# Kernel optimization log

Measured on AMD Instinct MI355X. Metric: run time of the kernel, lower is better.

## Reference

```python
import jax, jax.numpy as jnp
import numpy as np

B, N, M = 8, 4096, 4096

def _sqdist(x, y):
    # x: [B,N,3], y: [B,M,3] -> squared euclidean distances [B,N,M]
    return jnp.sum((x[:, :, None, :] - y[:, None, :, :]) ** 2, axis=-1)

def _approx_match(xyz1, xyz2):
    # Faithful port of Fan et al. approxmatch.cu (used by PyTorchEMD's
    # earth_mover_distance): annealed soft-assignment over 10 levels.
    b, n, _ = xyz1.shape
    m = xyz2.shape[1]
    d2 = _sqdist(xyz1, xyz2)                      # [B,N,M]
    factorl = max(n, m) / n
    factorr = max(n, m) / m
    satl = jnp.full((b, n), factorl, d2.dtype)    # remaining mass, left
    satr = jnp.full((b, m), factorr, d2.dtype)    # remaining mass, right
    match = jnp.zeros_like(d2)
    # levels: -4^7 .. -4^-1, then 0 (exactly as in approxmatch.cu)
    levels = [-(4.0 ** j) for j in range(7, -2, -1)] + [0.0]
    for level in levels:
        w = jnp.exp(level * d2) * satr[:, None, :]                 # [B,N,M]
        w = w * (satl / (jnp.sum(w, axis=2) + 1e-9))[:, :, None]   # row normalize
        ss2 = jnp.sum(w, axis=1)                                   # [B,M]
        ratio = jnp.minimum(satr / (ss2 + 1e-9), 1.0)
        w = w * ratio[:, None, :]                                  # col capacity clamp
        match = match + w
        satl = jnp.maximum(satl - jnp.sum(w, axis=2), 0.0)
        satr = jnp.maximum(satr - ss2 * ratio, 0.0)
    return match, d2

def setup_inputs() -> dict:
    key = jax.random.key(0)
    k1, k2 = jax.random.split(key)
    array1 = jax.random.uniform(k1, (B, N, 3), dtype=jnp.float32)
    array2 = jax.random.uniform(k2, (B, M, 3), dtype=jnp.float32)
    return {"array1": array1, "array2": array2}

def reference(array1, array2):
    match, d2 = _approx_match(array1, array2)
    dist = jnp.sum(match * d2, axis=(1, 2))   # per-batch EMD (squared-dist transport cost), [B]
    return jnp.mean(dist) / array1.shape[1]
```

## Files before the change

kernel.cpp:

```cpp
#include <hip/hip_runtime.h>


#define BB 8
#define NN 4096
#define MM 4096
#define NPTS 4096

constexpr int BLK   = 256;
constexpr int S     = 16;
constexpr int R     = 4;
constexpr int RPB   = (BLK / S) * R;
constexpr int CHUNK = 2048;
constexpr int G     = (CHUNK / S) / 4;

#if defined(__has_builtin)
#if __has_builtin(__builtin_amdgcn_exp2f)
#define EXP2F(x) __builtin_amdgcn_exp2f(x)
#endif
#if __has_builtin(__builtin_amdgcn_logf)
#define LOG2F(x) __builtin_amdgcn_logf(x)
#endif
#endif
#ifndef EXP2F
#define EXP2F(x) exp2f(x)
#endif
#ifndef LOG2F
#define LOG2F(x) log2f(x)
#endif

__global__ void emd_sort(const float* __restrict__ xyz, float* __restrict__ xyzs) {
    __shared__ int hist[64];
    __shared__ int offs[64];
    __shared__ int cur[64];
    const int b = blockIdx.x;
    const float* src = xyz + (size_t)b * NPTS * 3;
    float* dst = xyzs + (size_t)b * NPTS * 3;
    for (int i = threadIdx.x; i < 64; i += BLK) hist[i] = 0;
    __syncthreads();
    for (int i = threadIdx.x; i < NPTS; i += BLK) {
        float x = src[3*i], y = src[3*i+1], z = src[3*i+2];
        int cx = (int)(x * 4.0f); cx = cx < 0 ? 0 : (cx > 3 ? 3 : cx);
        int cy = (int)(y * 4.0f); cy = cy < 0 ? 0 : (cy > 3 ? 3 : cy);
        int cz = (int)(z * 4.0f); cz = cz < 0 ? 0 : (cz > 3 ? 3 : cz);
        atomicAdd(&hist[(cx << 4) | (cy << 2) | cz], 1);
    }
    __syncthreads();
    if (threadIdx.x == 0) {
        int acc = 0;
        for (int k = 0; k < 64; ++k) { offs[k] = acc; cur[k] = acc; acc += hist[k]; }
    }
    __syncthreads();
    for (int i = threadIdx.x; i < NPTS; i += BLK) {
        float x = src[3*i], y = src[3*i+1], z = src[3*i+2];
        int cx = (int)(x * 4.0f); cx = cx < 0 ? 0 : (cx > 3 ? 3 : cx);
        int cy = (int)(y * 4.0f); cy = cy < 0 ? 0 : (cy > 3 ? 3 : cy);
        int cz = (int)(z * 4.0f); cz = cz < 0 ? 0 : (cz > 3 ? 3 : cz);
        int idx = atomicAdd(&cur[(cx << 4) | (cy << 2) | cz], 1);
        dst[3*idx] = x; dst[3*idx+1] = y; dst[3*idx+2] = z;
    }
}

__global__ void emd_bbox(const float* __restrict__ xyzs, float* __restrict__ bb,
                         int gp) {
    const int grp = blockIdx.x, lane = threadIdx.x;
    float xlo = 1e30f, xhi = -1e30f, ylo = 1e30f, yhi = -1e30f,
          zlo = 1e30f, zhi = -1e30f;
    if (lane < gp) {
        const float* p = xyzs + ((size_t)grp * gp + lane) * 3;
        xlo = xhi = p[0]; ylo = yhi = p[1]; zlo = zhi = p[2];
    }
    #pragma unroll
    for (int d = 1; d < 64; d <<= 1) {
        xlo = fminf(xlo, __shfl_xor(xlo, d)); xhi = fmaxf(xhi, __shfl_xor(xhi, d));
        ylo = fminf(ylo, __shfl_xor(ylo, d)); yhi = fmaxf(yhi, __shfl_xor(yhi, d));
        zlo = fminf(zlo, __shfl_xor(zlo, d)); zhi = fmaxf(zhi, __shfl_xor(zhi, d));
    }
    if (lane == 0) {
        float* o = bb + (size_t)grp * 6;
        o[0]=xlo; o[1]=xhi; o[2]=ylo; o[3]=yhi; o[4]=zlo; o[5]=zhi;
    }
}

__global__ void emd_init(float* __restrict__ satl, float* __restrict__ satr,
                         float* __restrict__ bsum, float* __restrict__ slsum,
                         float* __restrict__ scal, float* __restrict__ out) {
    int i = blockIdx.x * blockDim.x + threadIdx.x;
    if (i < BB * NN) satl[i] = 1.0f;
    if (i < BB * MM) satr[i] = 1.0f;
    if (i < BB)      bsum[i] = 0.0f;
    if (i < BB)      slsum[i] = 0.0f;
    if (i < BB * 5)  scal[i] = 0.0f;
    if (i == 0)      out[0]  = 0.0f;
}

#define AB_LOAD(vv, gg)                                          \
    _Pragma("unroll")                                            \
    for (int k = 0; k < 4; ++k) vv[k] = q[((gg)*4 + k)*S + s];

#define AB_COMP(vv)                                              \
    _Pragma("unroll")                                            \
    for (int k = 0; k < 4; ++k) {                                \
        float4 v = vv[k];                                        \
        _Pragma("unroll")                                        \
        for (int r = 0; r < R; ++r) {                            \
            float a0 = v.w + cpp[r];                             \
            float a1 = fmaf(zs[r], v.z, a0);                     \
            float a2 = fmaf(ys[r], v.y, a1);                     \
            float arg = fmaf(xs[r], v.x, a2);                    \
            acc[r] += EXP2F(arg);                                \
        }                                                        \
    }

#define RED_S(v)                                                 \
    v += __shfl_xor(v, 1);  v += __shfl_xor(v, 2);               \
    v += __shfl_xor(v, 4);  v += __shfl_xor(v, 8);

#define RED_W(v)                                                 \
    v += __shfl_xor(v, 1);  v += __shfl_xor(v, 2);               \
    v += __shfl_xor(v, 4);  v += __shfl_xor(v, 8);               \
    v += __shfl_xor(v, 16); v += __shfl_xor(v, 32);

#define BOX_SETUP(rbb)                                           \
    const float* rb = (rbb) + (size_t)(b * 256 + tile * 4 + (threadIdx.x >> 6)) * 6; \
    const float rx0 = rb[0], rx1 = rb[1], ry0 = rb[2], ry1 = rb[3], \
                rz0 = rb[4], rz1 = rb[5];

#define BOX_D2M(cbb, c0, gs, d2m)                                \
    const float* cb = (cbb) + (size_t)(b * 64 + ((c0) >> 6) + (gs)) * 6; \
    float gx = fmaxf(0.0f, fmaxf(cb[0] - rx1, rx0 - cb[1]));     \
    float gy = fmaxf(0.0f, fmaxf(cb[2] - ry1, ry0 - cb[3]));     \
    float gz = fmaxf(0.0f, fmaxf(cb[4] - rz1, rz0 - cb[5]));     \
    float d2m = fmaf(gx, gx, fmaf(gy, gy, gz * gz));

__global__ __launch_bounds__(BLK, 2) void emd_passA_p(
        const float* __restrict__ xyz1, const float* __restrict__ xyz2,
        const float* __restrict__ satl, const float* __restrict__ satr,
        float* __restrict__ sl, const float* __restrict__ rbb,
        const float* __restrict__ cbb, float c, float T) {
    __shared__ float4 q[CHUNK];
    const int b    = blockIdx.x / (NN / RPB);
    const int tile = blockIdx.x % (NN / RPB);
    const float* x2b = xyz2 + (size_t)b * MM * 3;
    const float* srb = satr + (size_t)b * MM;

    const int g = threadIdx.x / S, s = threadIdx.x % S;
    const int n0 = tile * RPB + g * R;
    const float* p = xyz1 + ((size_t)b * NN + n0) * 3;
    const float m2c = -2.0f * c;
    float xs[R], ys[R], zs[R], cpp[R], acc[R];
    #pragma unroll
    for (int r = 0; r < R; ++r) {
        float x = p[3*r], y = p[3*r+1], z = p[3*r+2];
        cpp[r] = c * (x*x + y*y + z*z);
        xs[r] = m2c * x; ys[r] = m2c * y; zs[r] = m2c * z;
        acc[r] = 0.0f;
    }
    BOX_SETUP(rbb);

    for (int c0 = 0; c0 < MM; c0 += CHUNK) {
        __syncthreads();
        for (int m = threadIdx.x; m < CHUNK; m += BLK) {
            int mm = c0 + m;
            float xx = x2b[3*mm], yy = x2b[3*mm+1], zz = x2b[3*mm+2];
            float qq = xx*xx + yy*yy + zz*zz;
            q[m] = make_float4(xx, yy, zz, fmaf(c, qq, LOG2F(srb[mm])));
        }
        __syncthreads();
        for (int gs = 0; gs < G; ++gs) {
            BOX_D2M(cbb, c0, gs, d2m);
            if (d2m > T) continue;
            float4 va[4];
            AB_LOAD(va, gs);
            AB_COMP(va);
        }
    }
    #pragma unroll
    for (int r = 0; r < R; ++r) { RED_S(acc[r]); }
    if (s == 0) {
        #pragma unroll
        for (int r = 0; r < R; ++r) {
            int gi = b * NN + n0 + r;
            sl[gi] = satl[gi] / (acc[r] + 1e-9f);
        }
    }
}

template<int PRUNE>
__global__ __launch_bounds__(BLK, 2) void emd_passB(
        const float* __restrict__ xyz1, const float* __restrict__ xyz2,
        const float* __restrict__ sl, float* __restrict__ satr,
        float* __restrict__ sr2, float* __restrict__ bsum,
        const float* __restrict__ rbb, const float* __restrict__ cbb,
        int do_sum, float c, float T) {
    __shared__ float4 q[CHUNK];
    const int b    = blockIdx.x / (MM / RPB);
    const int tile = blockIdx.x % (MM / RPB);
    const float* x1b = xyz1 + (size_t)b * NN * 3;
    const float* slb = sl + (size_t)b * NN;

    const int g = threadIdx.x / S, s = threadIdx.x % S;
    const int m0 = tile * RPB + g * R;
    const float* qp = xyz2 + ((size_t)b * MM + m0) * 3;
    const float m2c = -2.0f * c;
    float xs[R], ys[R], zs[R], cpp[R], acc[R];
    #pragma unroll
    for (int r = 0; r < R; ++r) {
        float x = qp[3*r], y = qp[3*r+1], z = qp[3*r+2];
        cpp[r] = c * (x*x + y*y + z*z);
        xs[r] = m2c * x; ys[r] = m2c * y; zs[r] = m2c * z;
        acc[r] = 0.0f;
    }
    BOX_SETUP(rbb);

    for (int c0 = 0; c0 < NN; c0 += CHUNK) {
        __syncthreads();
        for (int n = threadIdx.x; n < CHUNK; n += BLK) {
            int nn = c0 + n;
            float xx = x1b[3*nn], yy = x1b[3*nn+1], zz = x1b[3*nn+2];
            float pp = xx*xx + yy*yy + zz*zz;
            q[n] = make_float4(xx, yy, zz, fmaf(c, pp, LOG2F(slb[nn])));
        }
        __syncthreads();
        if (PRUNE) {
            for (int gs = 0; gs < G; ++gs) {
                BOX_D2M(cbb, c0, gs, d2m);
                if (d2m > T) continue;
                float4 va[4];
                AB_LOAD(va, gs);
                AB_COMP(va);
            }
        } else {
            float4 va[4], vb[4];
            AB_LOAD(va, 0);
            #pragma unroll 1
            for (int gs = 0; gs < G; gs += 2) {
                AB_LOAD(vb, gs + 1);
                AB_COMP(va);
                if (gs + 2 < G) { AB_LOAD(va, gs + 2); }
                AB_COMP(vb);
            }
        }
    }
    #pragma unroll
    for (int r = 0; r < R; ++r) { RED_S(acc[r]); }
    float part = 0.0f;
    if (s == 0) {
        #pragma unroll
        for (int r = 0; r < R; ++r) {
            int gi = b * MM + m0 + r;
            float sr    = satr[gi];
            float ss2   = acc[r] * sr;
            float ratio = fminf(sr / (ss2 + 1e-9f), 1.0f);
            float sn    = fmaxf(sr - ss2 * ratio, 0.0f);
            sr2[gi]  = sr * ratio;
            satr[gi] = sn;
            part += sn;
        }
    }
    if (do_sum) {
        RED_W(part);
        if ((threadIdx.x & 63) == 0) atomicAdd(&bsum[b], part);
    }
}

#define CA0_LOAD(vv, ww, gg)                                     \
    _Pragma("unroll")                                            \
    for (int k = 0; k < 4; ++k) {                                \
        int idx = ((gg)*4 + k)*S + s;                            \
        vv[k] = q[idx]; ww[k] = w[idx];                          \
    }

#define CA0_COMP(vv, ww)                                         \
    _Pragma("unroll")                                            \
    for (int k = 0; k < 4; ++k) {                                \
        float4 v = vv[k]; float2 wv = ww[k];                     \
        _Pragma("unroll")                                        \
        for (int r = 0; r < R; ++r) {                            \
            float a0 = v.w + cnpp[r];                            \
            float a1 = fmaf(zs[r], v.z, a0);                     \
            float a2 = fmaf(ys[r], v.y, a1);                     \
            float arg = fmaf(xs[r], v.x, a2);                    \
            float en  = EXP2F(arg);                              \
            acc2[r] = fmaf(en, wv.y, acc2[r]);                   \
            float e2 = en * en;                                  \
            float t  = (e2 * e2) * wv.x;                         \
            rd[r]   += t;                                        \
            costA[r] = fmaf(t, arg, costA[r]);                   \
        }                                                        \
    }

template<int PRUNE>
__global__ __launch_bounds__(BLK, 2) void emd_passCA0(
        const float* __restrict__ xyz1, const float* __restrict__ xyz2,
        float* __restrict__ sl, float* __restrict__ satl,
        const float* __restrict__ sr2, const float* __restrict__ satr_next,
        float* __restrict__ out, const float* __restrict__ rbb,
        const float* __restrict__ cbb, float cl, float cn, float T) {
    __shared__ float4 q[CHUNK];
    __shared__ float2 w[CHUNK];
    const int b    = blockIdx.x / (NN / RPB);
    const int tile = blockIdx.x % (NN / RPB);
    const float* x2b = xyz2 + (size_t)b * MM * 3;
    const float* s2b = sr2 + (size_t)b * MM;
    const float* srb = satr_next + (size_t)b * MM;

    const int g = threadIdx.x / S, s = threadIdx.x % S;
    const int n0 = tile * RPB + g * R;
    const float* pp_ = xyz1 + ((size_t)b * NN + n0) * 3;
    const float m2cn = -2.0f * cn;
    const float icn  = 1.0f / cn;
    float xs[R], ys[R], zs[R], cnpp[R], rd[R], costA[R], acc2[R], slv[R];
    #pragma unroll
    for (int r = 0; r < R; ++r) {
        float x = pp_[3*r], y = pp_[3*r+1], z = pp_[3*r+2];
        cnpp[r] = cn * (x*x + y*y + z*z);
        xs[r] = m2cn * x; ys[r] = m2cn * y; zs[r] = m2cn * z;
        rd[r] = 0.0f; costA[r] = 0.0f; acc2[r] = 0.0f;
        slv[r] = sl[b * NN + n0 + r];
    }
    BOX_SETUP(rbb);

    for (int c0 = 0; c0 < MM; c0 += CHUNK) {
        __syncthreads();
        for (int m = threadIdx.x; m < CHUNK; m += BLK) {
            int mm = c0 + m;
            float xx = x2b[3*mm], yy = x2b[3*mm+1], zz = x2b[3*mm+2];
            float qq = xx*xx + yy*yy + zz*zz;
            q[m] = make_float4(xx, yy, zz, cn * qq);
            w[m] = make_float2(s2b[mm], srb[mm]);
        }
        __syncthreads();

        if (PRUNE) {
            for (int gs = 0; gs < G; ++gs) {
                BOX_D2M(cbb, c0, gs, d2m);
                if (d2m > T) continue;
                float4 va[4]; float2 wa[4];
                CA0_LOAD(va, wa, gs);
                CA0_COMP(va, wa);
            }
        } else {
            float4 va[4], vb[4]; float2 wa[4], wb[4];
            CA0_LOAD(va, wa, 0);
            #pragma unroll 1
            for (int gs = 0; gs < G; gs += 2) {
                CA0_LOAD(vb, wb, gs + 1);
                CA0_COMP(va, wa);
                if (gs + 2 < G) { CA0_LOAD(va, wa, gs + 2); }
                CA0_COMP(vb, wb);
            }
        }
    }

    #pragma unroll
    for (int r = 0; r < R; ++r) { RED_S(rd[r]); RED_S(acc2[r]); }

    float csum = 0.0f;
    #pragma unroll
    for (int r = 0; r < R; ++r) csum += (costA[r] * icn) * slv[r];
    RED_W(csum);
    if ((threadIdx.x & 63) == 0)
        atomicAdd(out, csum * (1.0f / (float)(BB * NN)));

    if (s == 0) {
        #pragma unroll
        for (int r = 0; r < R; ++r) {
            int gi = b * NN + n0 + r;
            float sa = fmaxf(satl[gi] - rd[r] * slv[r], 0.0f);
            satl[gi] = sa;
            sl[gi] = sa / (acc2[r] + 1e-9f);
        }
    }
}

#define CA1_LOAD(vv, aa, gg)                                     \
    _Pragma("unroll")                                            \
    for (int k = 0; k < 4; ++k) {                                \
        int idx = ((gg)*4 + k)*S + s;                            \
        vv[k] = q[idx]; aa[k] = qa[idx];                         \
    }

#define CA1_COMP(vv, aa)                                         \
    _Pragma("unroll")                                            \
    for (int k = 0; k < 4; ++k) {                                \
        float4 v = vv[k]; float lw = aa[k];                      \
        _Pragma("unroll")                                        \
        for (int r = 0; r < R; ++r) {                            \
            float a0 = v.w + clpp[r];                            \
            float a1 = fmaf(zs[r], v.z, a0);                     \
            float a2 = fmaf(ys[r], v.y, a1);                     \
            float arg = fmaf(xs[r], v.x, a2);                    \
            float t   = EXP2F(arg);                              \
            rd[r] += t;                                          \
            c1[r] = fmaf(t, arg, c1[r]);                         \
            c2[r] = fmaf(t, lw, c2[r]);                          \
        }                                                        \
    }

__global__ __launch_bounds__(BLK, 2) void emd_passCA1(
        const float* __restrict__ xyz1, const float* __restrict__ xyz2,
        float* __restrict__ sl, float* __restrict__ satl,
        const float* __restrict__ sr2, const float* __restrict__ bsum,
        float* __restrict__ slsum, float* __restrict__ out, float cl) {
    __shared__ float4 q[CHUNK];
    __shared__ float  qa[CHUNK];
    const int b    = blockIdx.x / (NN / RPB);
    const int tile = blockIdx.x % (NN / RPB);
    const float* x2b = xyz2 + (size_t)b * MM * 3;
    const float* s2b = sr2 + (size_t)b * MM;

    const int g = threadIdx.x / S, s = threadIdx.x % S;
    const int n0 = tile * RPB + g * R;
    const float* pp_ = xyz1 + ((size_t)b * NN + n0) * 3;
    const float m2cl = -2.0f * cl;
    const float icl  = 1.0f / cl;
    float xs[R], ys[R], zs[R], clpp[R], rd[R], c1[R], c2[R], slv[R];
    #pragma unroll
    for (int r = 0; r < R; ++r) {
        float x = pp_[3*r], y = pp_[3*r+1], z = pp_[3*r+2];
        clpp[r] = cl * (x*x + y*y + z*z);
        xs[r] = m2cl * x; ys[r] = m2cl * y; zs[r] = m2cl * z;
        rd[r] = 0.0f; c1[r] = 0.0f; c2[r] = 0.0f;
        slv[r] = sl[b * NN + n0 + r];
    }

    for (int c0 = 0; c0 < MM; c0 += CHUNK) {
        __syncthreads();
        for (int m = threadIdx.x; m < CHUNK; m += BLK) {
            int mm = c0 + m;
            float xx = x2b[3*mm], yy = x2b[3*mm+1], zz = x2b[3*mm+2];
            float qq = xx*xx + yy*yy + zz*zz;
            float lw = LOG2F(fmaxf(s2b[mm], 1e-30f));
            q[m]  = make_float4(xx, yy, zz, fmaf(cl, qq, lw));
            qa[m] = lw;
        }
        __syncthreads();

        float4 va[4], vb[4]; float aa[4], ab[4];
        CA1_LOAD(va, aa, 0);
        #pragma unroll 1
        for (int gs = 0; gs < G; gs += 2) {
            CA1_LOAD(vb, ab, gs + 1);
            CA1_COMP(va, aa);
            if (gs + 2 < G) { CA1_LOAD(va, aa, gs + 2); }
            CA1_COMP(vb, ab);
        }
    }

    #pragma unroll
    for (int r = 0; r < R; ++r) { RED_S(rd[r]); }

    float csum = 0.0f;
    #pragma unroll
    for (int r = 0; r < R; ++r) csum += ((c1[r] - c2[r]) * icl) * slv[r];
    RED_W(csum);
    if ((threadIdx.x & 63) == 0)
        atomicAdd(out, csum * (1.0f / (float)(BB * NN)));

    float part = 0.0f;
    if (s == 0) {
        float bs = bsum[b];
        #pragma unroll
        for (int r = 0; r < R; ++r) {
            int gi = b * NN + n0 + r;
            float sa = fmaxf(satl[gi] - rd[r] * slv[r], 0.0f);
            satl[gi] = sa;
            float s9 = sa / (bs + 1e-9f);
            sl[gi] = s9;
            part += s9;
        }
    }
    RED_W(part);
    if ((threadIdx.x & 63) == 0) atomicAdd(&slsum[b], part);
}

__global__ void emd_lvl9_col(const float* __restrict__ xyz2,
                             const float* __restrict__ satr,
                             const float* __restrict__ slsum,
                             float* __restrict__ scal) {
    int i = blockIdx.x * blockDim.x + threadIdx.x;
    int b = i / MM;
    const float* qp = xyz2 + (size_t)i * 3;
    float sr = satr[i];
    float ss2 = sr * slsum[b];
    float ratio = fminf(sr / (ss2 + 1e-9f), 1.0f);
    float s2 = sr * ratio;
    float x = qp[0], y = qp[1], z = qp[2];
    float v0 = s2, v1 = s2*x, v2 = s2*y, v3 = s2*z;
    float v4 = s2 * (x*x + y*y + z*z);
    #pragma unroll
    for (int d = 1; d < 64; d <<= 1) {
        v0 += __shfl_xor(v0, d); v1 += __shfl_xor(v1, d);
        v2 += __shfl_xor(v2, d); v3 += __shfl_xor(v3, d);
        v4 += __shfl_xor(v4, d);
    }
    if ((threadIdx.x & 63) == 0) {
        atomicAdd(&scal[b*5+0], v0); atomicAdd(&scal[b*5+1], v1);
        atomicAdd(&scal[b*5+2], v2); atomicAdd(&scal[b*5+3], v3);
        atomicAdd(&scal[b*5+4], v4);
    }
}

__global__ void emd_lvl9_cost(const float* __restrict__ xyz1,
                              const float* __restrict__ sl,
                              const float* __restrict__ scal,
                              float* __restrict__ out) {
    int i = blockIdx.x * blockDim.x + threadIdx.x;
    int b = i / NN;
    float W  = scal[b*5+0], Wx = scal[b*5+1], Wy = scal[b*5+2];
    float Wz = scal[b*5+3], Q  = scal[b*5+4];
    const float* p = xyz1 + (size_t)i * 3;
    float x = p[0], y = p[1], z = p[2];
    float pp = x*x + y*y + z*z;
    float dotw = x*Wx + y*Wy + z*Wz;
    float c = sl[i] * (pp * W + Q - 2.0f * dotw);
    #pragma unroll
    for (int d = 1; d < 64; d <<= 1) c += __shfl_xor(c, d);
    if ((threadIdx.x & 63) == 0)
        atomicAdd(out, c * (1.0f / (float)(BB * NN)));
}

extern "C" void kernel_launch(void* const* d_in, const int* in_sizes, int n_in,
                              void* d_out, int out_size, void* d_ws, size_t ws_size,
                              hipStream_t stream) {
    const float* xyz1 = (const float*)d_in[0];
    const float* xyz2 = (const float*)d_in[1];
    float* out  = (float*)d_out;

    float* satl  = (float*)d_ws;
    float* sl    = satl  + BB * NN;
    float* satr  = sl    + BB * NN;
    float* sr2   = satr  + BB * MM;
    float* bsum  = sr2   + BB * MM;
    float* slsum = bsum  + BB;
    float* scal  = slsum + BB;
    float* xyz1s = scal  + BB * 5;
    float* xyz2s = xyz1s + BB * NN * 3;
    float* bb1_16 = xyz2s + BB * MM * 3;
    float* bb1_64 = bb1_16 + BB * 256 * 6;
    float* bb2_16 = bb1_64 + BB * 64 * 6;
    float* bb2_64 = bb2_16 + BB * 256 * 6;

    emd_sort<<<BB, BLK, 0, stream>>>(xyz1, xyz1s);
    emd_sort<<<BB, BLK, 0, stream>>>(xyz2, xyz2s);
    emd_bbox<<<BB * (NN / 16), 64, 0, stream>>>(xyz1s, bb1_16, 16);
    emd_bbox<<<BB * (NN / 64), 64, 0, stream>>>(xyz1s, bb1_64, 64);
    emd_bbox<<<BB * (MM / 16), 64, 0, stream>>>(xyz2s, bb2_16, 16);
    emd_bbox<<<BB * (MM / 64), 64, 0, stream>>>(xyz2s, bb2_64, 64);
    emd_init<<<(BB * NN + 255) / 256, 256, 0, stream>>>(satl, satr, bsum,
                                                        slsum, scal, out);

    const double levels[10] = {-16384.0, -4096.0, -1024.0, -256.0, -64.0,
                               -16.0, -4.0, -1.0, -0.25, 0.0};
    const double LOG2E = 1.4426950408889634;
    float c[10], T[10];
    for (int l = 0; l < 10; ++l) {
        c[l] = (float)(levels[l] * LOG2E);
        T[l] = (l < 9) ? (float)(80.0 / (-levels[l] * LOG2E)) : 1e30f;
    }

    const int grid = BB * (NN / RPB);

    emd_passA_p<<<grid, BLK, 0, stream>>>(xyz1s, xyz2s, satl, satr, sl,
                                          bb1_16, bb2_64, c[0], T[0]);
    for (int l = 0; l <= 8; ++l) {
        if (l <= 3)
            emd_passB<1><<<grid, BLK, 0, stream>>>(
                xyz1s, xyz2s, sl, satr, sr2, bsum, bb2_16, bb1_64, 0, c[l], T[l]);
        else
            emd_passB<0><<<grid, BLK, 0, stream>>>(
                xyz1s, xyz2s, sl, satr, sr2, bsum, bb2_16, bb1_64,
                (l == 8) ? 1 : 0, c[l], 1e30f);
        if (l <= 2)
            emd_passCA0<1><<<grid, BLK, 0, stream>>>(
                xyz1s, xyz2s, sl, satl, sr2, satr, out, bb1_16, bb2_64,
                c[l], c[l + 1], T[l + 1]);
        else if (l < 8)
            emd_passCA0<0><<<grid, BLK, 0, stream>>>(
                xyz1s, xyz2s, sl, satl, sr2, satr, out, bb1_16, bb2_64,
                c[l], c[l + 1], 1e30f);
        else
            emd_passCA1<<<grid, BLK, 0, stream>>>(
                xyz1s, xyz2s, sl, satl, sr2, bsum, slsum, out, c[l]);
    }
    emd_lvl9_col<<<BB * MM / 256, 256, 0, stream>>>(xyz2s, satr, slsum, scal);
    emd_lvl9_cost<<<BB * NN / 256, 256, 0, stream>>>(xyz1s, sl, scal, out);
}
```

Measured before the change: 856.6 us.

## Compact saturated rows and columns out of the dense annealing levels

Adds compaction kernels that gather the points whose remaining mass is above a small threshold into packed float4 buffers with index maps. Levels 3 to 8 then run new passB/passCA0/passCA1 variants over only the active rows and columns, and blocks past the active count return early. Nearly-saturated points contribute almost no work, so this aims to cut the O(N·M) exp work in the later levels. In exchange it adds two compaction launches per level, indirect scatter writes, and a small approximation from treating mass below 1e-8 as zero.

```diff
diff --git a/kernel.cpp b/kernel.cpp
--- a/kernel.cpp
+++ b/kernel.cpp
@@ -6,12 +6,13 @@
 #define MM 4096
 #define NPTS 4096
 
-constexpr int BLK   = 256;
-constexpr int S     = 16;
-constexpr int R     = 4;
-constexpr int RPB   = (BLK / S) * R;
-constexpr int CHUNK = 2048;
-constexpr int G     = (CHUNK / S) / 4;
+constexpr int   BLK   = 256;
+constexpr int   S     = 16;
+constexpr int   R     = 4;
+constexpr int   RPB   = (BLK / S) * R;
+constexpr int   CHUNK = 2048;
+constexpr int   G     = (CHUNK / S) / 4;
+constexpr float TAU   = 1e-8f;
 
 #if defined(__has_builtin)
 #if __has_builtin(__builtin_amdgcn_exp2f)
@@ -30,7 +31,6 @@
 
 __global__ void emd_sort(const float* __restrict__ xyz, float* __restrict__ xyzs) {
     __shared__ int hist[64];
-    __shared__ int offs[64];
     __shared__ int cur[64];
     const int b = blockIdx.x;
     const float* src = xyz + (size_t)b * NPTS * 3;
@@ -47,7 +47,7 @@
     __syncthreads();
     if (threadIdx.x == 0) {
         int acc = 0;
-        for (int k = 0; k < 64; ++k) { offs[k] = acc; cur[k] = acc; acc += hist[k]; }
+        for (int k = 0; k < 64; ++k) { cur[k] = acc; acc += hist[k]; }
     }
     __syncthreads();
     for (int i = threadIdx.x; i < NPTS; i += BLK) {
@@ -91,6 +91,88 @@
     if (i < BB)      slsum[i] = 0.0f;
     if (i < BB * 5)  scal[i] = 0.0f;
     if (i == 0)      out[0]  = 0.0f;
+}
+
+__global__ void compact_rows(const float* __restrict__ xyzs,
+                             const float* __restrict__ satl,
+                             float* __restrict__ sl,
+                             float4* __restrict__ rowBuf, int* __restrict__ rIdx,
+                             int* __restrict__ rCnt) {
+    __shared__ int cnts[BLK];
+    const int b = blockIdx.x;
+    const int PER = NN / BLK;
+    const float* sb  = satl + (size_t)b * NN;
+    float*       slb = sl   + (size_t)b * NN;
+    const float* xb  = xyzs + (size_t)b * NN * 3;
+    const int st = threadIdx.x * PER;
+    int c = 0;
+    for (int i = 0; i < PER; ++i) c += (sb[st + i] > TAU) ? 1 : 0;
+    cnts[threadIdx.x] = c;
+    __syncthreads();
+    for (int d = 1; d < BLK; d <<= 1) {
+        int v = cnts[threadIdx.x];
+        int u = (threadIdx.x >= d) ? cnts[threadIdx.x - d] : 0;
+        __syncthreads();
+        cnts[threadIdx.x] = v + u;
+        __syncthreads();
+    }
+    const int total = cnts[BLK - 1];
+    int off = cnts[threadIdx.x] - c;
+    for (int i = 0; i < PER; ++i) {
+        int n = st + i;
+        if (sb[n] > TAU) {
+            rowBuf[(size_t)b * NN + off] =
+                make_float4(xb[3*n], xb[3*n+1], xb[3*n+2], slb[n]);
+            rIdx[(size_t)b * NN + off] = n;
+            ++off;
+        } else if (slb[n] != 0.0f) {
+            slb[n] = 0.0f;
+        }
+    }
+    for (int i = total + threadIdx.x; i < NN; i += BLK) {
+        rowBuf[(size_t)b * NN + i] = make_float4(0.f, 0.f, 0.f, 0.f);
+        rIdx[(size_t)b * NN + i] = 0;
+    }
+    if (threadIdx.x == 0) rCnt[b] = total;
+}
+
+__global__ void compact_cols(const float* __restrict__ xyzs,
+                             const float* __restrict__ satr,
+                             float4* __restrict__ colBuf, int* __restrict__ cIdx,
+                             int* __restrict__ cCnt) {
+    __shared__ int cnts[BLK];
+    const int b = blockIdx.x;
+    const int PER = MM / BLK;
+    const float* sb = satr + (size_t)b * MM;
+    const float* xb = xyzs + (size_t)b * MM * 3;
+    const int st = threadIdx.x * PER;
+    int c = 0;
+    for (int i = 0; i < PER; ++i) c += (sb[st + i] > TAU) ? 1 : 0;
+    cnts[threadIdx.x] = c;
+    __syncthreads();
+    for (int d = 1; d < BLK; d <<= 1) {
+        int v = cnts[threadIdx.x];
+        int u = (threadIdx.x >= d) ? cnts[threadIdx.x - d] : 0;
+        __syncthreads();
+        cnts[threadIdx.x] = v + u;
+        __syncthreads();
+    }
+    const int total = cnts[BLK - 1];
+    int off = cnts[threadIdx.x] - c;
+    for (int i = 0; i < PER; ++i) {
+        int m = st + i;
+        if (sb[m] > TAU) {
+            colBuf[(size_t)b * MM + off] =
+                make_float4(xb[3*m], xb[3*m+1], xb[3*m+2], sb[m]);
+            cIdx[(size_t)b * MM + off] = m;
+            ++off;
+        }
+    }
+    for (int i = total + threadIdx.x; i < MM; i += BLK) {
+        colBuf[(size_t)b * MM + i] = make_float4(0.f, 0.f, 0.f, 0.f);
+        cIdx[(size_t)b * MM + i] = 0;
+    }
+    if (threadIdx.x == 0) cCnt[b] = total;
 }
 
 #define AB_LOAD(vv, gg)                                          \
@@ -185,13 +267,11 @@
     }
 }
 
-template<int PRUNE>
-__global__ __launch_bounds__(BLK, 2) void emd_passB(
+__global__ __launch_bounds__(BLK, 2) void emd_passB_p(
         const float* __restrict__ xyz1, const float* __restrict__ xyz2,
         const float* __restrict__ sl, float* __restrict__ satr,
-        float* __restrict__ sr2, float* __restrict__ bsum,
-        const float* __restrict__ rbb, const float* __restrict__ cbb,
-        int do_sum, float c, float T) {
+        float* __restrict__ sr2, const float* __restrict__ rbb,
+        const float* __restrict__ cbb, float c, float T) {
     __shared__ float4 q[CHUNK];
     const int b    = blockIdx.x / (MM / RPB);
     const int tile = blockIdx.x % (MM / RPB);
@@ -221,29 +301,16 @@
             q[n] = make_float4(xx, yy, zz, fmaf(c, pp, LOG2F(slb[nn])));
         }
         __syncthreads();
-        if (PRUNE) {
-            for (int gs = 0; gs < G; ++gs) {
-                BOX_D2M(cbb, c0, gs, d2m);
-                if (d2m > T) continue;
-                float4 va[4];
-                AB_LOAD(va, gs);
-                AB_COMP(va);
-            }
-        } else {
-            float4 va[4], vb[4];
-            AB_LOAD(va, 0);
-            #pragma unroll 1
-            for (int gs = 0; gs < G; gs += 2) {
-                AB_LOAD(vb, gs + 1);
-                AB_COMP(va);
-                if (gs + 2 < G) { AB_LOAD(va, gs + 2); }
-                AB_COMP(vb);
-            }
+        for (int gs = 0; gs < G; ++gs) {
+            BOX_D2M(cbb, c0, gs, d2m);
+            if (d2m > T) continue;
+            float4 va[4];
+            AB_LOAD(va, gs);
+            AB_COMP(va);
         }
     }
     #pragma unroll
     for (int r = 0; r < R; ++r) { RED_S(acc[r]); }
-    float part = 0.0f;
     if (s == 0) {
         #pragma unroll
         for (int r = 0; r < R; ++r) {
@@ -254,12 +321,7 @@
             float sn    = fmaxf(sr - ss2 * ratio, 0.0f);
             sr2[gi]  = sr * ratio;
             satr[gi] = sn;
-            part += sn;
-        }
-    }
-    if (do_sum) {
-        RED_W(part);
-        if ((threadIdx.x & 63) == 0) atomicAdd(&bsum[b], part);
+        }
     }
 }
 
@@ -289,8 +351,7 @@
         }                                                        \
     }
 
-template<int PRUNE>
-__global__ __launch_bounds__(BLK, 2) void emd_passCA0(
+__global__ __launch_bounds__(BLK, 2) void emd_passCA0_p(
         const float* __restrict__ xyz1, const float* __restrict__ xyz2,
         float* __restrict__ sl, float* __restrict__ satl,
         const float* __restrict__ sr2, const float* __restrict__ satr_next,
@@ -330,25 +391,12 @@
             w[m] = make_float2(s2b[mm], srb[mm]);
         }
         __syncthreads();
-
-        if (PRUNE) {
-            for (int gs = 0; gs < G; ++gs) {
-                BOX_D2M(cbb, c0, gs, d2m);
-                if (d2m > T) continue;
-                float4 va[4]; float2 wa[4];
-                CA0_LOAD(va, wa, gs);
-                CA0_COMP(va, wa);
-            }
-        } else {
-            float4 va[4], vb[4]; float2 wa[4], wb[4];
-            CA0_LOAD(va, wa, 0);
-            #pragma unroll 1
-            for (int gs = 0; gs < G; gs += 2) {
-                CA0_LOAD(vb, wb, gs + 1);
-                CA0_COMP(va, wa);
-                if (gs + 2 < G) { CA0_LOAD(va, wa, gs + 2); }
-                CA0_COMP(vb, wb);
-            }
+        for (int gs = 0; gs < G; ++gs) {
+            BOX_D2M(cbb, c0, gs, d2m);
+            if (d2m > T) continue;
+            float4 va[4]; float2 wa[4];
+            CA0_LOAD(va, wa, gs);
+            CA0_COMP(va, wa);
         }
     }
 
@@ -369,6 +417,167 @@
             float sa = fmaxf(satl[gi] - rd[r] * slv[r], 0.0f);
             satl[gi] = sa;
             sl[gi] = sa / (acc2[r] + 1e-9f);
+        }
+    }
+}
+
+__global__ __launch_bounds__(BLK, 2) void emd_passB_c(
+        const float4* __restrict__ colBuf, const int* __restrict__ cIdx,
+        const int* __restrict__ cCnt, const float4* __restrict__ rowBuf,
+        const int* __restrict__ rCnt, float* __restrict__ satr,
+        float* __restrict__ sr2c, float* __restrict__ satrnc,
+        float* __restrict__ bsum, int do_sum, float c) {
+    __shared__ float4 q[CHUNK];
+    const int b    = blockIdx.x / (MM / RPB);
+    const int tile = blockIdx.x % (MM / RPB);
+    const int Mc = cCnt[b], Nc = rCnt[b];
+    if (tile * RPB >= Mc) return;
+    const float4* rb = rowBuf + (size_t)b * NN;
+
+    const int g = threadIdx.x / S, s = threadIdx.x % S;
+    const int m0 = tile * RPB + g * R;
+    const float m2c = -2.0f * c;
+    float xs[R], ys[R], zs[R], cpp[R], acc[R], srv[R];
+    #pragma unroll
+    for (int r = 0; r < R; ++r) {
+        float4 cv = colBuf[(size_t)b * MM + m0 + r];
+        srv[r] = cv.w;
+        cpp[r] = c * (cv.x*cv.x + cv.y*cv.y + cv.z*cv.z);
+        xs[r] = m2c * cv.x; ys[r] = m2c * cv.y; zs[r] = m2c * cv.z;
+        acc[r] = 0.0f;
+    }
+
+    const int nch = (Nc + CHUNK - 1) / CHUNK;
+    for (int ci = 0; ci < nch; ++ci) {
+        const int c0 = ci * CHUNK;
+        __syncthreads();
+        for (int n = threadIdx.x; n < CHUNK; n += BLK) {
+            int nn = c0 + n;
+            if (nn < Nc) {
+                float4 rv = rb[nn];
+                float pp = rv.x*rv.x + rv.y*rv.y + rv.z*rv.z;
+                q[n] = make_float4(rv.x, rv.y, rv.z, fmaf(c, pp, LOG2F(rv.w)));
+            } else {
+                q[n] = make_float4(0.f, 0.f, 0.f, -1e30f);
+            }
+        }
+        __syncthreads();
+        int rem = Nc - c0; if (rem > CHUNK) rem = CHUNK;
+        const int Gact = (rem + S*4 - 1) / (S*4);
+        float4 va[4], vb[4];
+        AB_LOAD(va, 0);
+        #pragma unroll 1
+        for (int gs = 0; gs < Gact; gs += 2) {
+            if (gs + 1 < Gact) { AB_LOAD(vb, gs + 1); }
+            AB_COMP(va);
+            if (gs + 2 < Gact) { AB_LOAD(va, gs + 2); }
+            if (gs + 1 < Gact) { AB_COMP(vb); }
+        }
+    }
+    #pragma unroll
+    for (int r = 0; r < R; ++r) { RED_S(acc[r]); }
+    float part = 0.0f;
+    if (s == 0) {
+        #pragma unroll
+        for (int r = 0; r < R; ++r) {
+            if (m0 + r < Mc) {
+                float sr    = srv[r];
+                float ss2   = acc[r] * sr;
+                float ratio = fminf(sr / (ss2 + 1e-9f), 1.0f);
+                float sn    = fmaxf(sr - ss2 * ratio, 0.0f);
+                size_t ci2 = (size_t)b * MM + m0 + r;
+                sr2c[ci2]   = sr * ratio;
+                satrnc[ci2] = sn;
+                satr[(size_t)b * MM + cIdx[ci2]] = sn;
+                part += sn;
+            }
+        }
+    }
+    if (do_sum) {
+        RED_W(part);
+        if ((threadIdx.x & 63) == 0) atomicAdd(&bsum[b], part);
+    }
+}
+
+__global__ __launch_bounds__(BLK, 2) void emd_passCA0_c(
+        const float4* __restrict__ rowBuf, const int* __restrict__ rIdx,
+        const int* __restrict__ rCnt, const float4* __restrict__ colBuf,
+        const int* __restrict__ cCnt, const float* __restrict__ sr2c,
+        const float* __restrict__ satrnc, float* __restrict__ satl,
+        float* __restrict__ sl, float* __restrict__ out, float cl, float cn) {
+    __shared__ float4 q[CHUNK];
+    __shared__ float2 w[CHUNK];
+    const int b    = blockIdx.x / (NN / RPB);
+    const int tile = blockIdx.x % (NN / RPB);
+    const int Nc = rCnt[b], Mc = cCnt[b];
+    if (tile * RPB >= Nc) return;
+    const float4* cbp = colBuf + (size_t)b * MM;
+    const float* s2p = sr2c + (size_t)b * MM;
+    const float* snp = satrnc + (size_t)b * MM;
+
+    const int g = threadIdx.x / S, s = threadIdx.x % S;
+    const int n0 = tile * RPB + g * R;
+    const float m2cn = -2.0f * cn;
+    const float icn  = 1.0f / cn;
+    float xs[R], ys[R], zs[R], cnpp[R], rd[R], costA[R], acc2[R], slv[R];
+    #pragma unroll
+    for (int r = 0; r < R; ++r) {
+        float4 rv = rowBuf[(size_t)b * NN + n0 + r];
+        slv[r] = rv.w;
+        cnpp[r] = cn * (rv.x*rv.x + rv.y*rv.y + rv.z*rv.z);
+        xs[r] = m2cn * rv.x; ys[r] = m2cn * rv.y; zs[r] = m2cn * rv.z;
+        rd[r] = 0.0f; costA[r] = 0.0f; acc2[r] = 0.0f;
+    }
+
+    const int nch = (Mc + CHUNK - 1) / CHUNK;
+    for (int ci = 0; ci < nch; ++ci) {
+        const int c0 = ci * CHUNK;
+        __syncthreads();
+        for (int m = threadIdx.x; m < CHUNK; m += BLK) {
+            int mm = c0 + m;
+            if (mm < Mc) {
+                float4 cv = cbp[mm];
+                float qq = cv.x*cv.x + cv.y*cv.y + cv.z*cv.z;
+                q[m] = make_float4(cv.x, cv.y, cv.z, cn * qq);
+                w[m] = make_float2(s2p[mm], snp[mm]);
+            } else {
+                q[m] = make_float4(0.f, 0.f, 0.f, 0.f);
+                w[m] = make_float2(0.f, 0.f);
+            }
+        }
+        __syncthreads();
+        int rem = Mc - c0; if (rem > CHUNK) rem = CHUNK;
+        const int Gact = (rem + S*4 - 1) / (S*4);
+        float4 va[4], vb[4]; float2 wa[4], wb[4];
+        CA0_LOAD(va, wa, 0);
+        #pragma unroll 1
+        for (int gs = 0; gs < Gact; gs += 2) {
+            if (gs + 1 < Gact) { CA0_LOAD(vb, wb, gs + 1); }
+            CA0_COMP(va, wa);
+            if (gs + 2 < Gact) { CA0_LOAD(va, wa, gs + 2); }
+            if (gs + 1 < Gact) { CA0_COMP(vb, wb); }
+        }
+    }
+
+    #pragma unroll
+    for (int r = 0; r < R; ++r) { RED_S(rd[r]); RED_S(acc2[r]); }
+
+    float csum = 0.0f;
+    #pragma unroll
+    for (int r = 0; r < R; ++r) csum += (costA[r] * icn) * slv[r];
+    RED_W(csum);
+    if ((threadIdx.x & 63) == 0)
+        atomicAdd(out, csum * (1.0f / (float)(BB * NN)));
+
+    if (s == 0) {
+        #pragma unroll
+        for (int r = 0; r < R; ++r) {
+            if (n0 + r < Nc) {
+                int gi = b * NN + rIdx[(size_t)b * NN + n0 + r];
+                float sa = fmaxf(satl[gi] - rd[r] * slv[r], 0.0f);
+                satl[gi] = sa;
+                sl[gi] = sa / (acc2[r] + 1e-9f);
+            }
         }
     }
 }
@@ -397,53 +606,64 @@
         }                                                        \
     }
 
-__global__ __launch_bounds__(BLK, 2) void emd_passCA1(
-        const float* __restrict__ xyz1, const float* __restrict__ xyz2,
-        float* __restrict__ sl, float* __restrict__ satl,
-        const float* __restrict__ sr2, const float* __restrict__ bsum,
-        float* __restrict__ slsum, float* __restrict__ out, float cl) {
+__global__ __launch_bounds__(BLK, 2) void emd_passCA1_c(
+        const float4* __restrict__ rowBuf, const int* __restrict__ rIdx,
+        const int* __restrict__ rCnt, const float4* __restrict__ colBuf,
+        const int* __restrict__ cCnt, const float* __restrict__ sr2c,
+        float* __restrict__ satl, float* __restrict__ sl,
+        const float* __restrict__ bsum, float* __restrict__ slsum,
+        float* __restrict__ out, float cl) {
     __shared__ float4 q[CHUNK];
     __shared__ float  qa[CHUNK];
     const int b    = blockIdx.x / (NN / RPB);
     const int tile = blockIdx.x % (NN / RPB);
-    const float* x2b = xyz2 + (size_t)b * MM * 3;
-    const float* s2b = sr2 + (size_t)b * MM;
+    const int Nc = rCnt[b], Mc = cCnt[b];
+    if (tile * RPB >= Nc) return;
+    const float4* cbp = colBuf + (size_t)b * MM;
+    const float* s2p = sr2c + (size_t)b * MM;
 
     const int g = threadIdx.x / S, s = threadIdx.x % S;
     const int n0 = tile * RPB + g * R;
-    const float* pp_ = xyz1 + ((size_t)b * NN + n0) * 3;
     const float m2cl = -2.0f * cl;
     const float icl  = 1.0f / cl;
     float xs[R], ys[R], zs[R], clpp[R], rd[R], c1[R], c2[R], slv[R];
     #pragma unroll
     for (int r = 0; r < R; ++r) {
-        float x = pp_[3*r], y = pp_[3*r+1], z = pp_[3*r+2];
-        clpp[r] = cl * (x*x + y*y + z*z);
-        xs[r] = m2cl * x; ys[r] = m2cl * y; zs[r] = m2cl * z;
+        float4 rv = rowBuf[(size_t)b * NN + n0 + r];
+        slv[r] = rv.w;
+        clpp[r] = cl * (rv.x*rv.x + rv.y*rv.y + rv.z*rv.z);
+        xs[r] = m2cl * rv.x; ys[r] = m2cl * rv.y; zs[r] = m2cl * rv.z;
         rd[r] = 0.0f; c1[r] = 0.0f; c2[r] = 0.0f;
-        slv[r] = sl[b * NN + n0 + r];
-    }
-
-    for (int c0 = 0; c0 < MM; c0 += CHUNK) {
+    }
+
+    const int nch = (Mc + CHUNK - 1) / CHUNK;
+    for (int ci = 0; ci < nch; ++ci) {
+        const int c0 = ci * CHUNK;
         __syncthreads();
         for (int m = threadIdx.x; m < CHUNK; m += BLK) {
             int mm = c0 + m;
-            float xx = x2b[3*mm], yy = x2b[3*mm+1], zz = x2b[3*mm+2];
-            float qq = xx*xx + yy*yy + zz*zz;
-            float lw = LOG2F(fmaxf(s2b[mm], 1e-30f));
-            q[m]  = make_float4(xx, yy, zz, fmaf(cl, qq, lw));
-            qa[m] = lw;
-        }
-        __syncthreads();
-
+            if (mm < Mc) {
+                float4 cv = cbp[mm];
+                float qq = cv.x*cv.x + cv.y*cv.y + cv.z*cv.z;
+                float lw = LOG2F(fmaxf(s2p[mm], 1e-30f));
+                q[m]  = make_float4(cv.x, cv.y, cv.z, fmaf(cl, qq, lw));
+                qa[m] = lw;
+            } else {
+                q[m]  = make_float4(0.f, 0.f, 0.f, -1e30f);
+                qa[m] = 0.f;
+            }
+        }
+        __syncthreads();
+        int rem = Mc - c0; if (rem > CHUNK) rem = CHUNK;
+        const int Gact = (rem + S*4 - 1) / (S*4);
         float4 va[4], vb[4]; float aa[4], ab[4];
         CA1_LOAD(va, aa, 0);
         #pragma unroll 1
-        for (int gs = 0; gs < G; gs += 2) {
-            CA1_LOAD(vb, ab, gs + 1);
+        for (int gs = 0; gs < Gact; gs += 2) {
+            if (gs + 1 < Gact) { CA1_LOAD(vb, ab, gs + 1); }
             CA1_COMP(va, aa);
-            if (gs + 2 < G) { CA1_LOAD(va, aa, gs + 2); }
-            CA1_COMP(vb, ab);
+            if (gs + 2 < Gact) { CA1_LOAD(va, aa, gs + 2); }
+            if (gs + 1 < Gact) { CA1_COMP(vb, ab); }
         }
     }
 
@@ -462,12 +682,14 @@
         float bs = bsum[b];
         #pragma unroll
         for (int r = 0; r < R; ++r) {
-            int gi = b * NN + n0 + r;
-            float sa = fmaxf(satl[gi] - rd[r] * slv[r], 0.0f);
-            satl[gi] = sa;
-            float s9 = sa / (bs + 1e-9f);
-            sl[gi] = s9;
-            part += s9;
+            if (n0 + r < Nc) {
+                int gi = b * NN + rIdx[(size_t)b * NN + n0 + r];
+                float sa = fmaxf(satl[gi] - rd[r] * slv[r], 0.0f);
+                satl[gi] = sa;
+                float s9 = sa / (bs + 1e-9f);
+                sl[gi] = s9;
+                part += s9;
+            }
         }
     }
     RED_W(part);
@@ -527,19 +749,27 @@
     const float* xyz2 = (const float*)d_in[1];
     float* out  = (float*)d_out;
 
-    float* satl  = (float*)d_ws;
-    float* sl    = satl  + BB * NN;
-    float* satr  = sl    + BB * NN;
-    float* sr2   = satr  + BB * MM;
-    float* bsum  = sr2   + BB * MM;
-    float* slsum = bsum  + BB;
-    float* scal  = slsum + BB;
-    float* xyz1s = scal  + BB * 5;
-    float* xyz2s = xyz1s + BB * NN * 3;
+    float* satl   = (float*)d_ws;
+    float* sl     = satl  + BB * NN;
+    float* satr   = sl    + BB * NN;
+    float* sr2    = satr  + BB * MM;
+    float* bsum   = sr2   + BB * MM;
+    float* slsum  = bsum  + BB;
+    float* scal   = slsum + BB;
+    float* xyz1s  = scal  + BB * 5;
+    float* xyz2s  = xyz1s + BB * NN * 3;
     float* bb1_16 = xyz2s + BB * MM * 3;
     float* bb1_64 = bb1_16 + BB * 256 * 6;
     float* bb2_16 = bb1_64 + BB * 64 * 6;
     float* bb2_64 = bb2_16 + BB * 256 * 6;
+    float4* rowBuf = (float4*)(bb2_64 + BB * 64 * 6);
+    float4* colBuf = rowBuf + BB * NN;
+    float* sr2c   = (float*)(colBuf + BB * MM);
+    float* satrnc = sr2c  + BB * MM;
+    int*   rIdx   = (int*)(satrnc + BB * MM);
+    int*   cIdx   = rIdx  + BB * NN;
+    int*   rCnt   = cIdx  + BB * MM;
+    int*   cCnt   = rCnt  + BB;
 
     emd_sort<<<BB, BLK, 0, stream>>>(xyz1, xyz1s);
     emd_sort<<<BB, BLK, 0, stream>>>(xyz2, xyz2s);
@@ -563,25 +793,31 @@
 
     emd_passA_p<<<grid, BLK, 0, stream>>>(xyz1s, xyz2s, satl, satr, sl,
                                           bb1_16, bb2_64, c[0], T[0]);
-    for (int l = 0; l <= 8; ++l) {
-        if (l <= 3)
-            emd_passB<1><<<grid, BLK, 0, stream>>>(
-                xyz1s, xyz2s, sl, satr, sr2, bsum, bb2_16, bb1_64, 0, c[l], T[l]);
-        else
-            emd_passB<0><<<grid, BLK, 0, stream>>>(
-                xyz1s, xyz2s, sl, satr, sr2, bsum, bb2_16, bb1_64,
-                (l == 8) ? 1 : 0, c[l], 1e30f);
-        if (l <= 2)
-            emd_passCA0<1><<<grid, BLK, 0, stream>>>(
-                xyz1s, xyz2s, sl, satl, sr2, satr, out, bb1_16, bb2_64,
-                c[l], c[l + 1], T[l + 1]);
-        else if (l < 8)
-            emd_passCA0<0><<<grid, BLK, 0, stream>>>(
-                xyz1s, xyz2s, sl, satl, sr2, satr, out, bb1_16, bb2_64,
-                c[l], c[l + 1], 1e30f);
-        else
-            emd_passCA1<<<grid, BLK, 0, stream>>>(
-                xyz1s, xyz2s, sl, satl, sr2, bsum, slsum, out, c[l]);
+    for (int l = 0; l <= 2; ++l) {
+        emd_passB_p<<<grid, BLK, 0, stream>>>(xyz1s, xyz2s, sl, satr, sr2,
+                                              bb2_16, bb1_64, c[l], T[l]);
+        emd_passCA0_p<<<grid, BLK, 0, stream>>>(
+            xyz1s, xyz2s, sl, satl, sr2, satr, out, bb1_16, bb2_64,
+            c[l], c[l + 1], T[l + 1]);
+    }
+
+    compact_cols<<<BB, BLK, 0, stream>>>(xyz2s, satr, colBuf, cIdx, cCnt);
+    compact_rows<<<BB, BLK, 0, stream>>>(xyz1s, satl, sl, rowBuf, rIdx, rCnt);
+    for (int l = 3; l <= 8; ++l) {
+        emd_passB_c<<<grid, BLK, 0, stream>>>(colBuf, cIdx, cCnt, rowBuf, rCnt,
+                                              satr, sr2c, satrnc, bsum,
+                                              (l == 8) ? 1 : 0, c[l]);
+        if (l < 8) {
+            emd_passCA0_c<<<grid, BLK, 0, stream>>>(
+                rowBuf, rIdx, rCnt, colBuf, cCnt, sr2c, satrnc,
+                satl, sl, out, c[l], c[l + 1]);
+            compact_cols<<<BB, BLK, 0, stream>>>(xyz2s, satr, colBuf, cIdx, cCnt);
+            compact_rows<<<BB, BLK, 0, stream>>>(xyz1s, satl, sl, rowBuf, rIdx, rCnt);
+        } else {
+            emd_passCA1_c<<<grid, BLK, 0, stream>>>(
+                rowBuf, rIdx, rCnt, colBuf, cCnt, sr2c,
+                satl, sl, bsum, slsum, out, c[8]);
+        }
     }
     emd_lvl9_col<<<BB * MM / 256, 256, 0, stream>>>(xyz2s, satr, slsum, scal);
     emd_lvl9_cost<<<BB * NN / 256, 256, 0, stream>>>(xyz1s, sl, scal, out);
```

Measured after the change: 775.4 us. -9.5%, faster.
